# Performance work log

Hardware: AMD Instinct MI355X
Metric: run time of the kernel (lower is better)

## Reference

```python
import jax, jax.numpy as jnp
import numpy as np

B, S, C, H, W, SHIFT = 8, 4096, 512, 16, 64, 32
HD = C // H        # head dim = 32
NW = S // W        # num windows = 64
EPS = 1e-5


def setup_inputs() -> dict:
    key = jax.random.key(0)
    ks = jax.random.split(key, 8)
    def n(k, shape, s=0.02):
        return jax.random.normal(k, shape, jnp.float32) * s
    return {
        "x": jax.random.normal(ks[0], (B, S, C), jnp.float32),
        "norm1_g": jnp.ones((C,), jnp.float32),
        "norm1_b": jnp.zeros((C,), jnp.float32),
        "qkv_w": n(ks[1], (3 * C, C)),
        "qkv_b": jnp.zeros((3 * C,), jnp.float32),
        "rel_bias": n(ks[2], (2 * W - 1, H)),
        "proj_w": n(ks[3], (C, C)),
        "proj_b": jnp.zeros((C,), jnp.float32),
        "norm2_g": jnp.ones((C,), jnp.float32),
        "norm2_b": jnp.zeros((C,), jnp.float32),
        "fc1_w": n(ks[4], (4 * C, C)),
        "fc1_b": jnp.zeros((4 * C,), jnp.float32),
        "fc2_w": n(ks[5], (C, 4 * C)),
        "fc2_b": jnp.zeros((C,), jnp.float32),
    }


def _layernorm(x, g, b):
    m = x.mean(-1, keepdims=True)
    v = ((x - m) ** 2).mean(-1, keepdims=True)
    return (x - m) * jax.lax.rsqrt(v + EPS) * g + b


def _attn_mask():
    # shifted-window mask, (NW, W, W) of {0, -100}
    seg = np.zeros(S, np.float32)
    seg[S - W: S - SHIFT] = 1.0
    seg[S - SHIFT:] = 2.0
    mw = seg.reshape(NW, W)
    d = mw[:, None, :] - mw[:, :, None]
    return jnp.asarray(np.where(d != 0, -100.0, 0.0).astype(np.float32))


def reference(x, norm1_g, norm1_b, qkv_w, qkv_b, rel_bias, proj_w, proj_b,
              norm2_g, norm2_b, fc1_w, fc1_b, fc2_w, fc2_b):
    # ---- W-MSA branch ----
    h = _layernorm(x, norm1_g, norm1_b)
    h = jnp.roll(h, -SHIFT, axis=1)                    # cyclic shift
    xw = h.reshape(B * NW, W, C)                       # window partition
    qkv = (xw @ qkv_w.T + qkv_b).reshape(B * NW, W, 3, H, HD)
    q, k, v = qkv[:, :, 0], qkv[:, :, 1], qkv[:, :, 2]  # (B_, W, H, HD)
    scale = HD ** -0.5
    attn = jnp.einsum('bnhd,bmhd->bhnm', q * scale, k)  # (B_, H, W, W)
    # relative position bias (1D): index = i - j + W - 1
    idx = jnp.arange(W)[:, None] - jnp.arange(W)[None, :] + (W - 1)
    bias = rel_bias[idx].transpose(2, 0, 1)             # (H, W, W)
    attn = attn + bias[None]
    attn = attn.reshape(B, NW, H, W, W) + _attn_mask()[None, :, None]
    attn = jax.nn.softmax(attn.reshape(B * NW, H, W, W), axis=-1)
    o = jnp.einsum('bhnm,bmhd->bnhd', attn, v).reshape(B * NW, W, C)
    o = o @ proj_w.T + proj_b
    o = o.reshape(B, S, C)
    o = jnp.roll(o, SHIFT, axis=1)                     # reverse cyclic shift
    x1 = x + o                                         # residual (drop_path = identity)
    # ---- MLP branch ----
    h2 = _layernorm(x1, norm2_g, norm2_b)
    h2 = jax.nn.gelu(h2 @ fc1_w.T + fc1_b, approximate=False)
    return x1 + (h2 @ fc2_w.T + fc2_b)
```

## Files before the change

### kernel.cpp

```cpp
#include <hip/hip_runtime.h>
#include <hip/hip_bf16.h>

typedef short short8 __attribute__((ext_vector_type(8)));
typedef short short4v __attribute__((ext_vector_type(4)));
typedef float f32x4 __attribute__((ext_vector_type(4)));

#define SHIFT_ 32

__device__ __forceinline__ float bf2f(unsigned short u) {
    union { unsigned int i; float f; } z; z.i = ((unsigned)u) << 16; return z.f;
}
__device__ __forceinline__ unsigned short f2bf(float f) {
    union { float f; unsigned int i; } z; z.f = f;
    unsigned int x = z.i;
    x += 0x7fffu + ((x >> 16) & 1u);
    return (unsigned short)(x >> 16);
}

__global__ __launch_bounds__(256)
void f2bf_kernel(const float* __restrict__ src, unsigned short* __restrict__ dst) {
    int i = (blockIdx.x * 256 + threadIdx.x) * 4;
    f32x4 v = *(const f32x4*)(src + i);
    short4v o;
#pragma unroll
    for (int j = 0; j < 4; j++) o[j] = (short)f2bf(v[j]);
    *(short4v*)(dst + i) = o;
}

__global__ __launch_bounds__(256)
void ln_kernel(const float* __restrict__ src,
               const float* __restrict__ gam,
               const float* __restrict__ bet,
               unsigned short* __restrict__ dst, int roll) {
    int wid = threadIdx.x >> 6, lane = threadIdx.x & 63;
    int m = (blockIdx.x << 2) + wid;
    int b = m >> 12, s = m & 4095;
    int ms = (b << 12) | ((s + roll) & 4095);
    const float* p = src + (size_t)ms * 512 + lane * 8;
    f32x4 v0 = *(const f32x4*)p;
    f32x4 v1 = *(const f32x4*)(p + 4);
    float f[8], sum = 0.f, sq = 0.f;
#pragma unroll
    for (int j = 0; j < 4; j++) { f[j] = v0[j]; f[j + 4] = v1[j]; }
#pragma unroll
    for (int j = 0; j < 8; j++) { sum += f[j]; sq += f[j] * f[j]; }
#pragma unroll
    for (int o = 1; o < 64; o <<= 1) { sum += __shfl_xor(sum, o); sq += __shfl_xor(sq, o); }
    float mean = sum * (1.f / 512.f);
    float rstd = rsqrtf(sq * (1.f / 512.f) - mean * mean + 1e-5f);
    const float* gp = gam + lane * 8;
    const float* bp = bet + lane * 8;
    f32x4 g0 = *(const f32x4*)gp, g1 = *(const f32x4*)(gp + 4);
    f32x4 b0 = *(const f32x4*)bp, b1 = *(const f32x4*)(bp + 4);
    short8 ov;
#pragma unroll
    for (int j = 0; j < 4; j++) {
        ov[j]     = (short)f2bf((f[j] - mean) * rstd * g0[j] + b0[j]);
        ov[j + 4] = (short)f2bf((f[j + 4] - mean) * rstd * g1[j] + b1[j]);
    }
    *(short8*)(dst + (size_t)m * 512 + lane * 8) = ov;
}

template <int N, int K, int EPI, bool OUTF32>
__global__ __launch_bounds__(256, 3)
void gemm_kernel(const unsigned short* __restrict__ A,
                 const unsigned short* __restrict__ Wt,
                 const float* __restrict__ bias,
                 void* __restrict__ outv,
                 const float* __restrict__ extraf, int nwg) {
    __shared__ __attribute__((aligned(16))) unsigned short sA[128 * 32];
    __shared__ __attribute__((aligned(16))) unsigned short sB[128 * 32];
    int cpx = nwg >> 3;
    int bid = (blockIdx.x & 7) * cpx + (blockIdx.x >> 3);
    const int nbx = N / 128;
    int bcol = bid % nbx, brow = bid / nbx;
    int m0 = brow << 7, n0 = bcol << 7;
    int t = threadIdx.x, lane = t & 63;
    int wr = (t >> 7) << 6;
    int wc = ((t >> 6) & 1) << 6;
    int rsel = lane & 15, ksel = (lane >> 4) << 3;

    f32x4 zero4 = {0.f, 0.f, 0.f, 0.f};
    f32x4 acc[4][4];
#pragma unroll
    for (int mi = 0; mi < 4; mi++)
#pragma unroll
        for (int ni = 0; ni < 4; ni++) acc[mi][ni] = zero4;

    for (int k0 = 0; k0 < K; k0 += 32) {
        __syncthreads();
#pragma unroll
        for (int i = 0; i < 2; i++) {
            int idx = t + (i << 8);
            int r = idx >> 2, co = (idx & 3) << 3;
            __builtin_amdgcn_global_load_lds(
                (const __attribute__((address_space(1))) void*)(A + (size_t)(m0 + r) * K + k0 + co),
                (__attribute__((address_space(3))) void*)(sA + idx * 8), 16, 0, 0);
            __builtin_amdgcn_global_load_lds(
                (const __attribute__((address_space(1))) void*)(Wt + (size_t)(n0 + r) * K + k0 + co),
                (__attribute__((address_space(3))) void*)(sB + idx * 8), 16, 0, 0);
        }
        __syncthreads();
        short8 af[4], bf[4];
#pragma unroll
        for (int mi = 0; mi < 4; mi++)
            af[mi] = *(const short8*)(sA + (wr + mi * 16 + rsel) * 32 + ksel);
#pragma unroll
        for (int ni = 0; ni < 4; ni++)
            bf[ni] = *(const short8*)(sB + (wc + ni * 16 + rsel) * 32 + ksel);
#pragma unroll
        for (int mi = 0; mi < 4; mi++)
#pragma unroll
            for (int ni = 0; ni < 4; ni++)
                acc[mi][ni] = __builtin_amdgcn_mfma_f32_16x16x32_bf16(af[mi], bf[ni], acc[mi][ni], 0, 0, 0);
    }

    int jbase = (lane >> 4) << 2;
#pragma unroll
    for (int ni = 0; ni < 4; ni++) {
        int gcol = n0 + wc + ni * 16 + rsel;
        float bv = bias[gcol];
#pragma unroll
        for (int mi = 0; mi < 4; mi++) {
#pragma unroll
            for (int j = 0; j < 4; j++) {
                int grow = m0 + wr + mi * 16 + jbase + j;
                float v = acc[mi][ni][j] + bv;
                size_t oidx;
                if (EPI == 2) {
                    int orow = (grow & ~4095) | ((grow + SHIFT_) & 4095);
                    oidx = (size_t)orow * N + gcol;
                    v += extraf[oidx];
                } else {
                    oidx = (size_t)grow * N + gcol;
                    if (EPI == 1) v = 0.5f * v * (1.f + erff(v * 0.70710678118654752f));
                    if (EPI == 3) v += extraf[oidx];
                }
                if (OUTF32) ((float*)outv)[oidx] = v;
                else        ((unsigned short*)outv)[oidx] = f2bf(v);
            }
        }
    }
}

__global__ __launch_bounds__(256, 2)
void attn_kernel(const unsigned short* __restrict__ qkv,
                 const float* __restrict__ relb,
                 unsigned short* __restrict__ obuf) {
    __shared__ __attribute__((aligned(16))) unsigned short Pl[4][64 * 72];
    __shared__ __attribute__((aligned(16))) unsigned short Vt[4][32 * 72];
    __shared__ float biasd[4][128];
    int wid = threadIdx.x >> 6, lane = threadIdx.x & 63;
    int task = (blockIdx.x << 2) + wid;
    int win = task >> 4, h = task & 15;
    const unsigned short* base = qkv + (size_t)win * 98304 + h * 32;

    float* bd = biasd[wid];
    bd[lane] = relb[lane * 16 + h];
    if (lane < 63) bd[lane + 64] = relb[(lane + 64) * 16 + h];

    int rsel = lane & 15, ksel = (lane >> 4) << 3;
    short8 qf[4], kf[4];
#pragma unroll
    for (int i = 0; i < 4; i++) {
        qf[i] = *(const short8*)(base + (size_t)(i * 16 + rsel) * 1536 + ksel);
        kf[i] = *(const short8*)(base + (size_t)(i * 16 + rsel) * 1536 + 512 + ksel);
    }
    f32x4 zero4 = {0.f, 0.f, 0.f, 0.f};
    f32x4 accS[4][4];
#pragma unroll
    for (int mi = 0; mi < 4; mi++)
#pragma unroll
        for (int ni = 0; ni < 4; ni++) accS[mi][ni] = zero4;
#pragma unroll
    for (int mi = 0; mi < 4; mi++)
#pragma unroll
        for (int ni = 0; ni < 4; ni++)
            accS[mi][ni] = __builtin_amdgcn_mfma_f32_16x16x32_bf16(qf[mi], kf[ni], accS[mi][ni], 0, 0, 0);

    unsigned short* vt = Vt[wid];
#pragma unroll 8
    for (int it = 0; it < 32; it++) {
        int idx = (it << 6) + lane;
        int vr = idx >> 5, vd = idx & 31;
        vt[vd * 72 + vr] = base[(size_t)vr * 1536 + 1024 + vd];
    }
    __syncthreads();

    const float scale = 0.17677669529663687f;
    bool masked = ((win & 63) == 63);
    int jbase = (lane >> 4) << 2;
    float rs[4][4];
#pragma unroll
    for (int mi = 0; mi < 4; mi++) {
#pragma unroll
        for (int ni = 0; ni < 4; ni++) {
            int colb = ni * 16 + rsel;
#pragma unroll
            for (int j = 0; j < 4; j++) {
                int row = mi * 16 + jbase + j;
                float v = accS[mi][ni][j] * scale + bd[row - colb + 63];
                if (masked && ((row < 32) != (colb < 32))) v -= 100.f;
                accS[mi][ni][j] = v;
            }
        }
#pragma unroll
        for (int j = 0; j < 4; j++) {
            float m = fmaxf(fmaxf(accS[mi][0][j], accS[mi][1][j]),
                            fmaxf(accS[mi][2][j], accS[mi][3][j]));
            m = fmaxf(m, __shfl_xor(m, 1));
            m = fmaxf(m, __shfl_xor(m, 2));
            m = fmaxf(m, __shfl_xor(m, 4));
            m = fmaxf(m, __shfl_xor(m, 8));
            float ssum = 0.f;
#pragma unroll
            for (int ni = 0; ni < 4; ni++) {
                float p = __expf(accS[mi][ni][j] - m);
                accS[mi][ni][j] = p; ssum += p;
            }
            ssum += __shfl_xor(ssum, 1);
            ssum += __shfl_xor(ssum, 2);
            ssum += __shfl_xor(ssum, 4);
            ssum += __shfl_xor(ssum, 8);
            rs[mi][j] = 1.f / ssum;
        }
    }
    unsigned short* pl = Pl[wid];
#pragma unroll
    for (int mi = 0; mi < 4; mi++)
#pragma unroll
        for (int ni = 0; ni < 4; ni++)
#pragma unroll
            for (int j = 0; j < 4; j++)
                pl[(mi * 16 + jbase + j) * 72 + ni * 16 + rsel] = f2bf(accS[mi][ni][j] * rs[mi][j]);
    __syncthreads();

    f32x4 accO[4][2];
#pragma unroll
    for (int mi = 0; mi < 4; mi++) { accO[mi][0] = zero4; accO[mi][1] = zero4; }
#pragma unroll
    for (int kk = 0; kk < 2; kk++) {
        short8 pa[4], vb[2];
#pragma unroll
        for (int mi = 0; mi < 4; mi++)
            pa[mi] = *(const short8*)(pl + (mi * 16 + rsel) * 72 + (kk << 5) + ksel);
#pragma unroll
        for (int ni = 0; ni < 2; ni++)
            vb[ni] = *(const short8*)(vt + (ni * 16 + rsel) * 72 + (kk << 5) + ksel);
#pragma unroll
        for (int mi = 0; mi < 4; mi++)
#pragma unroll
            for (int ni = 0; ni < 2; ni++)
                accO[mi][ni] = __builtin_amdgcn_mfma_f32_16x16x32_bf16(pa[mi], vb[ni], accO[mi][ni], 0, 0, 0);
    }
    unsigned short* op = obuf + (size_t)win * 32768 + h * 32;
#pragma unroll
    for (int mi = 0; mi < 4; mi++)
#pragma unroll
        for (int ni = 0; ni < 2; ni++)
#pragma unroll
            for (int j = 0; j < 4; j++)
                op[(size_t)(mi * 16 + jbase + j) * 512 + ni * 16 + rsel] = f2bf(accO[mi][ni][j]);
}

extern "C" void kernel_launch(void* const* d_in, const int* in_sizes, int n_in,
                              void* d_out, int out_size, void* d_ws, size_t ws_size,
                              hipStream_t stream) {
    (void)in_sizes; (void)n_in; (void)out_size; (void)ws_size;
    const float* x       = (const float*)d_in[0];
    const float* norm1_g = (const float*)d_in[1];
    const float* norm1_b = (const float*)d_in[2];
    const float* qkv_w   = (const float*)d_in[3];
    const float* qkv_b   = (const float*)d_in[4];
    const float* rel_b   = (const float*)d_in[5];
    const float* proj_w  = (const float*)d_in[6];
    const float* proj_b  = (const float*)d_in[7];
    const float* norm2_g = (const float*)d_in[8];
    const float* norm2_b = (const float*)d_in[9];
    const float* fc1_w   = (const float*)d_in[10];
    const float* fc1_b   = (const float*)d_in[11];
    const float* fc2_w   = (const float*)d_in[12];
    const float* fc2_b   = (const float*)d_in[13];

    char* ws = (char*)d_ws;
    unsigned short* hn   = (unsigned short*)(ws);
    unsigned short* qkvb = (unsigned short*)(ws + 33554432);
    unsigned short* obuf = hn;
    unsigned short* wq   = (unsigned short*)(ws + 167772160);
    unsigned short* wp   = (unsigned short*)(ws + 167772160 + 1572864);
    unsigned short* w1   = (unsigned short*)(ws + 167772160 + 1572864 + 524288);
    unsigned short* w2   = (unsigned short*)(ws + 167772160 + 1572864 + 524288 + 2097152);
    float* x1f           = (float*)d_out;
    float* outf          = (float*)d_out;

    f2bf_kernel<<<768, 256, 0, stream>>>(qkv_w, wq);
    f2bf_kernel<<<256, 256, 0, stream>>>(proj_w, wp);
    f2bf_kernel<<<1024, 256, 0, stream>>>(fc1_w, w1);
    f2bf_kernel<<<1024, 256, 0, stream>>>(fc2_w, w2);
    ln_kernel<<<8192, 256, 0, stream>>>(x, norm1_g, norm1_b, hn, SHIFT_);
    gemm_kernel<1536, 512, 0, false><<<3072, 256, 0, stream>>>(hn, wq, qkv_b, qkvb, nullptr, 3072);
    attn_kernel<<<2048, 256, 0, stream>>>(qkvb, rel_b, obuf);
    gemm_kernel<512, 512, 2, true><<<1024, 256, 0, stream>>>(obuf, wp, proj_b, x1f, x, 1024);
    ln_kernel<<<8192, 256, 0, stream>>>(x1f, norm2_g, norm2_b, hn, 0);
    gemm_kernel<2048, 512, 1, false><<<4096, 256, 0, stream>>>(hn, w1, fc1_b, qkvb, nullptr, 4096);
    gemm_kernel<512, 2048, 3, true><<<1024, 256, 0, stream>>>(qkvb, w2, fc2_b, outf, x1f, 1024);
}
```

Baseline: 439.4 us.

## Double-buffer GEMM shared-memory tiles to overlap global loads with MFMA

Result: slower. 456.5 us (+3.9%).

```diff
diff --git a/kernel.cpp b/kernel.cpp
--- a/kernel.cpp
+++ b/kernel.cpp
@@ -68,8 +68,8 @@
                  const float* __restrict__ bias,
                  void* __restrict__ outv,
                  const float* __restrict__ extraf, int nwg) {
-    __shared__ __attribute__((aligned(16))) unsigned short sA[128 * 32];
-    __shared__ __attribute__((aligned(16))) unsigned short sB[128 * 32];
+    __shared__ __attribute__((aligned(16))) unsigned short sA[2][128 * 32];
+    __shared__ __attribute__((aligned(16))) unsigned short sB[2][128 * 32];
     int cpx = nwg >> 3;
     int bid = (blockIdx.x & 7) * cpx + (blockIdx.x >> 3);
     const int nbx = N / 128;
@@ -80,6 +80,25 @@
     int wc = ((t >> 6) & 1) << 6;
     int rsel = lane & 15, ksel = (lane >> 4) << 3;
 
+    int r0 = t >> 2, c0 = (t & 3) << 3;
+    int r1 = (t + 256) >> 2, c1 = ((t + 256) & 3) << 3;
+
+#define STAGE(buf, k0)                                                                  \
+    do {                                                                                \
+        __builtin_amdgcn_global_load_lds(                                               \
+            (const __attribute__((address_space(1))) void*)(A + (size_t)(m0 + r0) * K + (k0) + c0), \
+            (__attribute__((address_space(3))) void*)(sA[buf] + t * 8), 16, 0, 0);      \
+        __builtin_amdgcn_global_load_lds(                                               \
+            (const __attribute__((address_space(1))) void*)(Wt + (size_t)(n0 + r0) * K + (k0) + c0), \
+            (__attribute__((address_space(3))) void*)(sB[buf] + t * 8), 16, 0, 0);      \
+        __builtin_amdgcn_global_load_lds(                                               \
+            (const __attribute__((address_space(1))) void*)(A + (size_t)(m0 + r1) * K + (k0) + c1), \
+            (__attribute__((address_space(3))) void*)(sA[buf] + (t + 256) * 8), 16, 0, 0); \
+        __builtin_amdgcn_global_load_lds(                                               \
+            (const __attribute__((address_space(1))) void*)(Wt + (size_t)(n0 + r1) * K + (k0) + c1), \
+            (__attribute__((address_space(3))) void*)(sB[buf] + (t + 256) * 8), 16, 0, 0); \
+    } while (0)
+
     f32x4 zero4 = {0.f, 0.f, 0.f, 0.f};
     f32x4 acc[4][4];
 #pragma unroll
@@ -87,33 +106,27 @@
 #pragma unroll
         for (int ni = 0; ni < 4; ni++) acc[mi][ni] = zero4;
 
+    STAGE(0, 0);
+    __syncthreads();
+    int cur = 0;
     for (int k0 = 0; k0 < K; k0 += 32) {
-        __syncthreads();
-#pragma unroll
-        for (int i = 0; i < 2; i++) {
-            int idx = t + (i << 8);
-            int r = idx >> 2, co = (idx & 3) << 3;
-            __builtin_amdgcn_global_load_lds(
-                (const __attribute__((address_space(1))) void*)(A + (size_t)(m0 + r) * K + k0 + co),
-                (__attribute__((address_space(3))) void*)(sA + idx * 8), 16, 0, 0);
-            __builtin_amdgcn_global_load_lds(
-                (const __attribute__((address_space(1))) void*)(Wt + (size_t)(n0 + r) * K + k0 + co),
-                (__attribute__((address_space(3))) void*)(sB + idx * 8), 16, 0, 0);
-        }
-        __syncthreads();
+        if (k0 + 32 < K) STAGE(cur ^ 1, k0 + 32);
         short8 af[4], bf[4];
 #pragma unroll
         for (int mi = 0; mi < 4; mi++)
-            af[mi] = *(const short8*)(sA + (wr + mi * 16 + rsel) * 32 + ksel);
+            af[mi] = *(const short8*)(sA[cur] + (wr + mi * 16 + rsel) * 32 + ksel);
 #pragma unroll
         for (int ni = 0; ni < 4; ni++)
-            bf[ni] = *(const short8*)(sB + (wc + ni * 16 + rsel) * 32 + ksel);
+            bf[ni] = *(const short8*)(sB[cur] + (wc + ni * 16 + rsel) * 32 + ksel);
 #pragma unroll
         for (int mi = 0; mi < 4; mi++)
 #pragma unroll
             for (int ni = 0; ni < 4; ni++)
                 acc[mi][ni] = __builtin_amdgcn_mfma_f32_16x16x32_bf16(af[mi], bf[ni], acc[mi][ni], 0, 0, 0);
-    }
+        __syncthreads();
+        cur ^= 1;
+    }
+#undef STAGE
 
     int jbase = (lane >> 4) << 2;
 #pragma unroll
```

## Enlarge GEMM tiles to 256x256 with double-buffered LDS and staged epilogue

Applied to the files above, without the earlier changes.

Result: slower. 565.0 us (+28.6%).

```diff
diff --git a/kernel.cpp b/kernel.cpp
--- a/kernel.cpp
+++ b/kernel.cpp
@@ -62,82 +62,142 @@
 }
 
 template <int N, int K, int EPI, bool OUTF32>
-__global__ __launch_bounds__(256, 3)
+__global__ __launch_bounds__(512, 2)
 void gemm_kernel(const unsigned short* __restrict__ A,
                  const unsigned short* __restrict__ Wt,
                  const float* __restrict__ bias,
                  void* __restrict__ outv,
                  const float* __restrict__ extraf, int nwg) {
-    __shared__ __attribute__((aligned(16))) unsigned short sA[128 * 32];
-    __shared__ __attribute__((aligned(16))) unsigned short sB[128 * 32];
+    __shared__ __attribute__((aligned(16))) unsigned short smem[65536];
     int cpx = nwg >> 3;
     int bid = (blockIdx.x & 7) * cpx + (blockIdx.x >> 3);
-    const int nbx = N / 128;
+    const int nbx = N / 256;
     int bcol = bid % nbx, brow = bid / nbx;
-    int m0 = brow << 7, n0 = bcol << 7;
+    int m0 = brow << 8, n0 = bcol << 8;
     int t = threadIdx.x, lane = t & 63;
-    int wr = (t >> 7) << 6;
-    int wc = ((t >> 6) & 1) << 6;
+    int w = t >> 6;
+    int wrm = w >> 2;
+    int wcn = w & 3;
     int rsel = lane & 15, ksel = (lane >> 4) << 3;
 
+    int srow[4], scoff[4];
+#pragma unroll
+    for (int i = 0; i < 4; i++) {
+        int c = i * 512 + t;
+        srow[i] = c >> 3; scoff[i] = (c & 7) << 3;
+    }
+
+#define BUFA(b) (smem + (b) * 32768)
+#define BUFB(b) (smem + (b) * 32768 + 16384)
+#define STAGE(buf, k0)                                                                     \
+    do {                                                                                   \
+        _Pragma("unroll")                                                                  \
+        for (int i = 0; i < 4; i++) {                                                      \
+            int c = i * 512 + t;                                                           \
+            __builtin_amdgcn_global_load_lds(                                              \
+                (const __attribute__((address_space(1))) void*)(A + (size_t)(m0 + srow[i]) * K + (k0) + scoff[i]), \
+                (__attribute__((address_space(3))) void*)(BUFA(buf) + c * 8), 16, 0, 0);   \
+            __builtin_amdgcn_global_load_lds(                                              \
+                (const __attribute__((address_space(1))) void*)(Wt + (size_t)(n0 + srow[i]) * K + (k0) + scoff[i]), \
+                (__attribute__((address_space(3))) void*)(BUFB(buf) + c * 8), 16, 0, 0);   \
+        }                                                                                  \
+    } while (0)
+
     f32x4 zero4 = {0.f, 0.f, 0.f, 0.f};
-    f32x4 acc[4][4];
-#pragma unroll
-    for (int mi = 0; mi < 4; mi++)
+    f32x4 acc[8][4];
+#pragma unroll
+    for (int mi = 0; mi < 8; mi++)
 #pragma unroll
         for (int ni = 0; ni < 4; ni++) acc[mi][ni] = zero4;
 
-    for (int k0 = 0; k0 < K; k0 += 32) {
+    STAGE(0, 0);
+    __syncthreads();
+    int cur = 0;
+    const int NT = K / 64;
+    for (int tt = 0; tt < NT; tt++) {
+        if (tt + 1 < NT) STAGE(cur ^ 1, (tt + 1) * 64);
+#pragma unroll
+        for (int kk = 0; kk < 2; kk++) {
+            short8 af[8], bf[4];
+#pragma unroll
+            for (int mi = 0; mi < 8; mi++)
+                af[mi] = *(const short8*)(BUFA(cur) + (wrm * 128 + mi * 16 + rsel) * 64 + kk * 32 + ksel);
+#pragma unroll
+            for (int ni = 0; ni < 4; ni++)
+                bf[ni] = *(const short8*)(BUFB(cur) + (wcn * 64 + ni * 16 + rsel) * 64 + kk * 32 + ksel);
+#pragma unroll
+            for (int mi = 0; mi < 8; mi++)
+#pragma unroll
+                for (int ni = 0; ni < 4; ni++)
+                    acc[mi][ni] = __builtin_amdgcn_mfma_f32_16x16x32_bf16(af[mi], bf[ni], acc[mi][ni], 0, 0, 0);
+        }
         __syncthreads();
-#pragma unroll
-        for (int i = 0; i < 2; i++) {
-            int idx = t + (i << 8);
-            int r = idx >> 2, co = (idx & 3) << 3;
-            __builtin_amdgcn_global_load_lds(
-                (const __attribute__((address_space(1))) void*)(A + (size_t)(m0 + r) * K + k0 + co),
-                (__attribute__((address_space(3))) void*)(sA + idx * 8), 16, 0, 0);
-            __builtin_amdgcn_global_load_lds(
-                (const __attribute__((address_space(1))) void*)(Wt + (size_t)(n0 + r) * K + k0 + co),
-                (__attribute__((address_space(3))) void*)(sB + idx * 8), 16, 0, 0);
-        }
-        __syncthreads();
-        short8 af[4], bf[4];
-#pragma unroll
-        for (int mi = 0; mi < 4; mi++)
-            af[mi] = *(const short8*)(sA + (wr + mi * 16 + rsel) * 32 + ksel);
-#pragma unroll
-        for (int ni = 0; ni < 4; ni++)
-            bf[ni] = *(const short8*)(sB + (wc + ni * 16 + rsel) * 32 + ksel);
-#pragma unroll
-        for (int mi = 0; mi < 4; mi++)
+        cur ^= 1;
+    }
+#undef STAGE
+#undef BUFA
+#undef BUFB
+
+    int jbase = (lane >> 4) << 2;
+#pragma unroll
+    for (int ni = 0; ni < 4; ni++) {
+        float bv = bias[n0 + wcn * 64 + ni * 16 + rsel];
+#pragma unroll
+        for (int mi = 0; mi < 8; mi++)
+#pragma unroll
+            for (int j = 0; j < 4; j++) {
+                float v = acc[mi][ni][j] + bv;
+                if (EPI == 1) v = 0.5f * v * (1.f + erff(v * 0.70710678118654752f));
+                acc[mi][ni][j] = v;
+            }
+    }
+
+    if (!OUTF32) {
+        unsigned short* eb = smem + w * 8192;
+#pragma unroll
+        for (int mi = 0; mi < 8; mi++)
 #pragma unroll
             for (int ni = 0; ni < 4; ni++)
-                acc[mi][ni] = __builtin_amdgcn_mfma_f32_16x16x32_bf16(af[mi], bf[ni], acc[mi][ni], 0, 0, 0);
-    }
-
-    int jbase = (lane >> 4) << 2;
-#pragma unroll
-    for (int ni = 0; ni < 4; ni++) {
-        int gcol = n0 + wc + ni * 16 + rsel;
-        float bv = bias[gcol];
-#pragma unroll
-        for (int mi = 0; mi < 4; mi++) {
-#pragma unroll
-            for (int j = 0; j < 4; j++) {
-                int grow = m0 + wr + mi * 16 + jbase + j;
-                float v = acc[mi][ni][j] + bv;
+#pragma unroll
+                for (int j = 0; j < 4; j++)
+                    eb[(mi * 16 + jbase + j) * 64 + ni * 16 + rsel] = f2bf(acc[mi][ni][j]);
+        unsigned short* outp = (unsigned short*)outv;
+#pragma unroll
+        for (int it = 0; it < 16; it++) {
+            int row = it * 8 + (lane >> 3), col = (lane & 7) << 3;
+            short8 vv = *(const short8*)(eb + row * 64 + col);
+            *(short8*)(outp + (size_t)(m0 + wrm * 128 + row) * N + n0 + wcn * 64 + col) = vv;
+        }
+    } else {
+        float* ebf = (float*)smem + w * 4096;
+        float* outp = (float*)outv;
+#pragma unroll
+        for (int h = 0; h < 2; h++) {
+#pragma unroll
+            for (int mi = 0; mi < 4; mi++)
+#pragma unroll
+                for (int ni = 0; ni < 4; ni++)
+#pragma unroll
+                    for (int j = 0; j < 4; j++)
+                        ebf[(mi * 16 + jbase + j) * 64 + ni * 16 + rsel] = acc[h * 4 + mi][ni][j];
+#pragma unroll
+            for (int it = 0; it < 16; it++) {
+                int row = it * 4 + (lane >> 4), c4 = (lane & 15) << 2;
+                f32x4 vv = *(const f32x4*)(ebf + row * 64 + c4);
+                int grow = m0 + wrm * 128 + h * 64 + row;
+                int gcol = n0 + wcn * 64 + c4;
                 size_t oidx;
                 if (EPI == 2) {
                     int orow = (grow & ~4095) | ((grow + SHIFT_) & 4095);
                     oidx = (size_t)orow * N + gcol;
-                    v += extraf[oidx];
                 } else {
                     oidx = (size_t)grow * N + gcol;
-                    if (EPI == 1) v = 0.5f * v * (1.f + erff(v * 0.70710678118654752f));
-                    if (EPI == 3) v += extraf[oidx];
                 }
-                if (OUTF32) ((float*)outv)[oidx] = v;
-                else        ((unsigned short*)outv)[oidx] = f2bf(v);
+                if (EPI == 2 || EPI == 3) {
+                    f32x4 ex = *(const f32x4*)(extraf + oidx);
+                    vv += ex;
+                }
+                *(f32x4*)(outp + oidx) = vv;
             }
         }
     }
@@ -298,10 +358,10 @@
     f2bf_kernel<<<1024, 256, 0, stream>>>(fc1_w, w1);
     f2bf_kernel<<<1024, 256, 0, stream>>>(fc2_w, w2);
     ln_kernel<<<8192, 256, 0, stream>>>(x, norm1_g, norm1_b, hn, SHIFT_);
-    gemm_kernel<1536, 512, 0, false><<<3072, 256, 0, stream>>>(hn, wq, qkv_b, qkvb, nullptr, 3072);
+    gemm_kernel<1536, 512, 0, false><<<768, 512, 0, stream>>>(hn, wq, qkv_b, qkvb, nullptr, 768);
     attn_kernel<<<2048, 256, 0, stream>>>(qkvb, rel_b, obuf);
-    gemm_kernel<512, 512, 2, true><<<1024, 256, 0, stream>>>(obuf, wp, proj_b, x1f, x, 1024);
+    gemm_kernel<512, 512, 2, true><<<256, 512, 0, stream>>>(obuf, wp, proj_b, x1f, x, 256);
     ln_kernel<<<8192, 256, 0, stream>>>(x1f, norm2_g, norm2_b, hn, 0);
-    gemm_kernel<2048, 512, 1, false><<<4096, 256, 0, stream>>>(hn, w1, fc1_b, qkvb, nullptr, 4096);
-    gemm_kernel<512, 2048, 3, true><<<1024, 256, 0, stream>>>(qkvb, w2, fc2_b, outf, x1f, 1024);
-}
+    gemm_kernel<2048, 512, 1, false><<<1024, 512, 0, stream>>>(hn, w1, fc1_b, qkvb, nullptr, 1024);
+    gemm_kernel<512, 2048, 3, true><<<256, 512, 0, stream>>>(qkvb, w2, fc2_b, outf, x1f, 256);
+}
```
